# Kernel tuning notes

Measured on AMD Instinct MI355X. Metric: run time of the kernel, lower is better.

Reference implementation:

```python
import jax, jax.numpy as jnp
import numpy as np

N, E, B = 30000, 480000, 64
F_IN, HID, ED = 128, 64, 32
NEG, EPS = 0.2, 1e-5


def _add_self_loops(edge_index, edge_attr):
    # PyG add_self_loops with fill_value='mean': self-loop edge_attr of node i
    # is the mean of edge_attr over edges whose destination is i.
    src, dst = edge_index[0], edge_index[1]
    cnt = jax.ops.segment_sum(jnp.ones((edge_attr.shape[0],), edge_attr.dtype), dst, num_segments=N)
    mean = jax.ops.segment_sum(edge_attr, dst, num_segments=N) / jnp.maximum(cnt, 1.0)[:, None]
    loop = jnp.arange(N)
    return jnp.concatenate([src, loop]), jnp.concatenate([dst, loop]), jnp.concatenate([edge_attr, mean], axis=0)


def _gat_conv(x, src, dst, ea, W, We, a_s, a_d, a_e, bias, H, Fo):
    xs = (x @ W).reshape(-1, H, Fo)              # [N, H, Fo]
    al_src = (xs * a_s).sum(-1)                  # [N, H]
    al_dst = (xs * a_d).sum(-1)                  # [N, H]
    ef = (ea @ We).reshape(-1, H, Fo)            # [Et, H, Fo]
    alpha = al_src[src] + al_dst[dst] + (ef * a_e).sum(-1)   # [Et, H]
    alpha = jax.nn.leaky_relu(alpha, NEG)
    # softmax over incoming edges of each destination node (segment softmax)
    m = jax.ops.segment_max(alpha, dst, num_segments=N)
    ex = jnp.exp(alpha - m[dst])
    s = jax.ops.segment_sum(ex, dst, num_segments=N)
    w = ex / s[dst]                              # [Et, H]
    out = jax.ops.segment_sum(xs[src] * w[:, :, None], dst, num_segments=N)
    return out.reshape(-1, H * Fo) + bias


def _bn(x, g, b):
    # BatchNorm1d in training mode: biased batch statistics over nodes
    mu = x.mean(0)
    var = x.var(0)
    return (x - mu) * jax.lax.rsqrt(var + EPS) * g + b


def _pool(x, batch, Wg, bg):
    # GlobalAttention: softmax(gate_nn(x)) per graph, weighted sum of x
    gate = (x @ Wg + bg)[:, 0]                   # [N]
    m = jax.ops.segment_max(gate, batch, num_segments=B)
    e = jnp.exp(gate - m[batch])
    s = jax.ops.segment_sum(e, batch, num_segments=B)
    w = e / s[batch]
    return jax.ops.segment_sum(x * w[:, None], batch, num_segments=B)   # [B, HID]


def setup_inputs():
    k = jax.random.split(jax.random.key(0), 16)
    g = lambda i, shape, fan: jax.random.normal(k[i], shape, jnp.float32) / np.sqrt(fan)
    return {
        "x": jax.random.normal(k[0], (N, F_IN), jnp.float32),
        "edge_attr": jax.random.normal(k[1], (E, ED), jnp.float32),
        "edge_index": jax.random.randint(k[2], (2, E), 0, N),
        "batch": jnp.sort(jax.random.randint(k[3], (N,), 0, B)),
        "W1": g(4, (F_IN, 4 * HID), F_IN),
        "We1": g(5, (ED, 4 * HID), ED),
        "att_src1": g(6, (4, HID), HID),
        "att_dst1": g(7, (4, HID), HID),
        "att_edge1": g(8, (4, HID), HID),
        "bias1": jnp.zeros((4 * HID,), jnp.float32),
        "g1": jnp.ones((4 * HID,), jnp.float32),
        "b1": jnp.zeros((4 * HID,), jnp.float32),
        "W2": g(9, (4 * HID, HID), 4 * HID),
        "We2": g(10, (ED, HID), ED),
        "att_src2": g(11, (1, HID), HID),
        "att_dst2": g(12, (1, HID), HID),
        "att_edge2": g(13, (1, HID), HID),
        "bias2": jnp.zeros((HID,), jnp.float32),
        "g2": jnp.ones((HID,), jnp.float32),
        "b2": jnp.zeros((HID,), jnp.float32),
        "Wg": g(14, (HID, 1), HID),
        "bg": jnp.zeros((1,), jnp.float32),
    }


def reference(x, edge_attr, edge_index, batch, W1, We1, att_src1, att_dst1, att_edge1, bias1, g1, b1, W2, We2, att_src2, att_dst2, att_edge2, bias2, g2, b2, Wg, bg):
    src, dst, ea = _add_self_loops(edge_index, edge_attr)
    h = jax.nn.relu(_bn(_gat_conv(x, src, dst, ea, W1, We1, att_src1, att_dst1, att_edge1, bias1, 4, HID), g1, b1))
    h = jax.nn.relu(_bn(_gat_conv(h, src, dst, ea, W2, We2, att_src2, att_dst2, att_edge2, bias2, 1, HID), g2, b2))
    return _pool(h, batch, Wg, bg)
```

## Files before the change

### kernel.cpp

```cpp
#include <hip/hip_runtime.h>
#include <math.h>

#define NN 30000
#define EE 480000
#define BB 64

typedef __bf16 b16x8 __attribute__((ext_vector_type(8)));
typedef float  f32x4 __attribute__((ext_vector_type(4)));
typedef unsigned short u16x8 __attribute__((ext_vector_type(8)));

__device__ __forceinline__ float wsum64(float v){
  #pragma unroll
  for (int m = 32; m >= 1; m >>= 1) v += __shfl_xor(v, m, 64);
  return v;
}
__device__ __forceinline__ float wmax64(float v){
  #pragma unroll
  for (int m = 32; m >= 1; m >>= 1) v = fmaxf(v, __shfl_xor(v, m, 64));
  return v;
}
__device__ __forceinline__ float wsum16(float v){
  #pragma unroll
  for (int m = 1; m < 16; m <<= 1) v += __shfl_xor(v, m, 64);
  return v;
}
__device__ __forceinline__ unsigned short f2b(float f){
  union { float f; unsigned u; } v; v.f = f;
  unsigned r = v.u + 0x7fffu + ((v.u >> 16) & 1u);
  return (unsigned short)(r >> 16);
}
__device__ __forceinline__ float b2f(unsigned short u){
  union { unsigned u; float f; } v; v.u = ((unsigned)u) << 16;
  return v.f;
}

__global__ void hist_kernel(const int* __restrict__ dst, int* __restrict__ deg){
  int e = blockIdx.x*256 + threadIdx.x;
  if (e < EE) atomicAdd(&deg[dst[e]], 1);
}

__global__ __launch_bounds__(256) void scan_kernel(const int* __restrict__ deg, int* __restrict__ rowptr){
  __shared__ int s[256];
  __shared__ int wred[4];
  const int b = blockIdx.x, tid = threadIdx.x;
  const int base = b*256;
  int part = 0;
  for (int idx = tid; idx < base; idx += 256) part += deg[idx];
  #pragma unroll
  for (int m = 32; m >= 1; m >>= 1) part += __shfl_xor(part, m, 64);
  if ((tid & 63) == 0) wred[tid >> 6] = part;
  __syncthreads();
  int offset = wred[0] + wred[1] + wred[2] + wred[3];
  int n = base + tid;
  int d = (n < NN) ? deg[n] : 0;
  s[tid] = d;
  __syncthreads();
  for (int off = 1; off < 256; off <<= 1){
    int v = (tid >= off) ? s[tid - off] : 0;
    __syncthreads();
    s[tid] += v;
    __syncthreads();
  }
  if (n < NN) rowptr[n] = offset + s[tid] - d;
  if (b == 0 && tid == 0) rowptr[NN] = EE;
}

__global__ void prep_kernel(const float* __restrict__ W1, const float* __restrict__ W2,
                            const float* __restrict__ We1, const float* __restrict__ ae1,
                            const float* __restrict__ We2, const float* __restrict__ ae2,
                            unsigned short* __restrict__ W1t, unsigned short* __restrict__ W2t,
                            float* __restrict__ wae){
  int t = threadIdx.x, b = blockIdx.x;
  if (b < 128){
    W1t[t*128 + b] = f2b(W1[b*256 + t]);
  } else if (b < 384){
    int k = b - 128;
    if (t < 64) W2t[t*256 + k] = f2b(W2[k*64 + t]);
  } else {
    if (t < 128){
      int h = t >> 5, k = t & 31;
      float s = 0.f;
      for (int f = 0; f < 64; f++) s += We1[k*256 + h*64 + f] * ae1[h*64 + f];
      wae[h*32 + k] = s;
    } else if (t < 160){
      int k = t - 128;
      float s = 0.f;
      for (int f = 0; f < 64; f++) s += We2[k*64 + f] * ae2[f];
      wae[128 + k] = s;
    }
  }
}

__global__ __launch_bounds__(256) void edge_kernel(const float* __restrict__ ea,
    const float* __restrict__ wae, const int* __restrict__ src, const int* __restrict__ dst,
    const int* __restrict__ rowptr, int* __restrict__ cursor,
    float* __restrict__ rec, float2* __restrict__ rec8){
  __shared__ float s_w[160];
  if (threadIdx.x < 160) s_w[threadIdx.x] = wae[threadIdx.x];
  __syncthreads();
  const int lane = threadIdx.x & 63;
  const int il = lane & 7;
  const int e = blockIdx.x*32 + (threadIdx.x >> 3);
  if (e >= EE) return;
  int slot = 0, sv = 0;
  if (il == 0){
    int dd = dst[e];
    slot = rowptr[dd] + atomicAdd(&cursor[dd], 1);
    sv = src[e];
  }
  float4 v = *(const float4*)(ea + (size_t)e*32 + il*4);
  float dots[5];
  #pragma unroll
  for (int h = 0; h < 5; h++){
    float4 w = *(const float4*)&s_w[h*32 + il*4];
    dots[h] = v.x*w.x + v.y*w.y + v.z*w.z + v.w*w.w;
  }
  #pragma unroll
  for (int m = 1; m < 8; m <<= 1)
    #pragma unroll
    for (int h = 0; h < 5; h++) dots[h] += __shfl_xor(dots[h], m, 64);
  slot = __shfl(slot, lane & ~7, 64);
  sv   = __shfl(sv,   lane & ~7, 64);
  if (il == 0){
    float4 lo; lo.x = dots[0]; lo.y = dots[1]; lo.z = dots[2]; lo.w = dots[3];
    *(float4*)(rec + (size_t)slot*8) = lo;
  } else if (il == 1){
    float4 hi; hi.x = dots[4]; hi.y = __int_as_float(sv); hi.z = 0.f; hi.w = 0.f;
    *(float4*)(rec + (size_t)slot*8 + 4) = hi;
  } else if (il == 2){
    float2 r8; r8.x = dots[4]; r8.y = __int_as_float(sv);
    rec8[slot] = r8;
  }
}

__global__ __launch_bounds__(256) void gemm1_mfma(const float* __restrict__ x,
    const unsigned short* __restrict__ Bt, const float* __restrict__ a_s, const float* __restrict__ a_d,
    unsigned short* __restrict__ out, float* __restrict__ alsrc, float* __restrict__ aldst){
  __shared__ unsigned short As[128*136];
  __shared__ unsigned short Bs[64*136];
  const int tid = threadIdx.x;
  const int w = tid >> 6, lane = tid & 63;
  const int c = lane & 15, gq = lane >> 4;
  const int m0 = blockIdx.x * 128;
  const int h0 = blockIdx.y * 2;
  #pragma unroll
  for (int q = 0; q < 16; q++){
    int ch = tid*16 + q;
    int r = ch >> 5, off = (ch & 31)*4;
    int grow = m0 + r;
    ushort4 o;
    if (grow < NN){
      float4 v = *(const float4*)(x + (size_t)grow*128 + off);
      o.x = f2b(v.x); o.y = f2b(v.y); o.z = f2b(v.z); o.w = f2b(v.w);
    } else o = make_ushort4(0,0,0,0);
    *(ushort4*)&As[r*136 + off] = o;
  }
  #pragma unroll
  for (int q = 0; q < 4; q++){
    int ch = tid*4 + q;
    int n = ch >> 4, off = (ch & 15)*8;
    *(ulonglong2*)&Bs[n*136 + off] = *(const ulonglong2*)(Bt + (size_t)(h0*64 + n)*128 + off);
  }
  __syncthreads();
  for (int hi = 0; hi < 2; hi++){
    const int head = h0 + hi;
    f32x4 acc[2][4];
    #pragma unroll
    for (int mt = 0; mt < 2; mt++)
      #pragma unroll
      for (int nt = 0; nt < 4; nt++) acc[mt][nt] = (f32x4){0.f,0.f,0.f,0.f};
    #pragma unroll
    for (int k0 = 0; k0 < 128; k0 += 32){
      b16x8 afr[2], bfr[4];
      #pragma unroll
      for (int mt = 0; mt < 2; mt++)
        afr[mt] = *(const b16x8*)&As[(w*32 + mt*16 + c)*136 + k0 + gq*8];
      #pragma unroll
      for (int nt = 0; nt < 4; nt++)
        bfr[nt] = *(const b16x8*)&Bs[(nt*16 + c)*136 + k0 + gq*8];
      #pragma unroll
      for (int mt = 0; mt < 2; mt++)
        #pragma unroll
        for (int nt = 0; nt < 4; nt++)
          acc[mt][nt] = __builtin_amdgcn_mfma_f32_16x16x32_bf16(afr[mt], bfr[nt], acc[mt][nt], 0, 0, 0);
    }
    __syncthreads();
    if (hi == 0){
      #pragma unroll
      for (int q = 0; q < 4; q++){
        int ch = tid*4 + q;
        int n = ch >> 4, off = (ch & 15)*8;
        *(ulonglong2*)&Bs[n*136 + off] = *(const ulonglong2*)(Bt + (size_t)((h0+1)*64 + n)*128 + off);
      }
    }
    float asv[4], adv[4];
    #pragma unroll
    for (int nt = 0; nt < 4; nt++){
      asv[nt] = a_s[head*64 + nt*16 + c];
      adv[nt] = a_d[head*64 + nt*16 + c];
    }
    #pragma unroll
    for (int mt = 0; mt < 2; mt++){
      int base_row = m0 + w*32 + mt*16 + gq*4;
      #pragma unroll
      for (int r = 0; r < 4; r++){
        int row = base_row + r;
        float ps = 0.f, pd = 0.f;
        #pragma unroll
        for (int nt = 0; nt < 4; nt++){
          ps += acc[mt][nt][r] * asv[nt];
          pd += acc[mt][nt][r] * adv[nt];
        }
        ps = wsum16(ps); pd = wsum16(pd);
        if (row < NN){
          if (c == 0){
            alsrc[(size_t)row*4 + head] = ps;
            aldst[(size_t)row*4 + head] = pd;
          }
          #pragma unroll
          for (int nt = 0; nt < 4; nt++)
            out[(size_t)row*256 + head*64 + nt*16 + c] = f2b(acc[mt][nt][r]);
        }
      }
    }
    if (hi == 0) __syncthreads();
  }
}

__global__ __launch_bounds__(256) void gemm2_mfma(const unsigned short* __restrict__ Ab,
    const unsigned short* __restrict__ Bt,
    const float* __restrict__ cs, const float* __restrict__ csq,
    const float* __restrict__ g, const float* __restrict__ b,
    const float* __restrict__ a_s, const float* __restrict__ a_d,
    unsigned short* __restrict__ out, float* __restrict__ alsrc, float* __restrict__ aldst){
  __shared__ unsigned short As[128*136];
  __shared__ unsigned short Bs[64*136];
  __shared__ float s_scale[256], s_shift[256];
  const int tid = threadIdx.x;
  const int w = tid >> 6, lane = tid & 63;
  const int c = lane & 15, gq = lane >> 4;
  const int m0 = blockIdx.x * 128;
  {
    float mu  = cs[tid]  * (1.f/NN);
    float var = csq[tid] * (1.f/NN) - mu*mu;
    float rs  = rsqrtf(var + 1e-5f);
    float sc  = rs * g[tid];
    s_scale[tid] = sc;
    s_shift[tid] = b[tid] - mu*sc;
  }
  __syncthreads();
  f32x4 acc[2][4];
  #pragma unroll
  for (int mt = 0; mt < 2; mt++)
    #pragma unroll
    for (int nt = 0; nt < 4; nt++) acc[mt][nt] = (f32x4){0.f,0.f,0.f,0.f};
  for (int kp = 0; kp < 256; kp += 128){
    #pragma unroll
    for (int q = 0; q < 16; q++){
      int ch = tid*16 + q;
      int r = ch >> 5, off = (ch & 31)*4;
      int grow = m0 + r;
      ushort4 o;
      if (grow < NN){
        ushort4 v = *(const ushort4*)(Ab + (size_t)grow*256 + kp + off);
        float4 sc = *(const float4*)&s_scale[kp + off];
        float4 sh = *(const float4*)&s_shift[kp + off];
        o.x = f2b(fmaxf(fmaf(b2f(v.x), sc.x, sh.x), 0.f));
        o.y = f2b(fmaxf(fmaf(b2f(v.y), sc.y, sh.y), 0.f));
        o.z = f2b(fmaxf(fmaf(b2f(v.z), sc.z, sh.z), 0.f));
        o.w = f2b(fmaxf(fmaf(b2f(v.w), sc.w, sh.w), 0.f));
      } else o = make_ushort4(0,0,0,0);
      *(ushort4*)&As[r*136 + off] = o;
    }
    #pragma unroll
    for (int q = 0; q < 4; q++){
      int ch = tid*4 + q;
      int n = ch >> 4, off = (ch & 15)*8;
      *(ulonglong2*)&Bs[n*136 + off] = *(const ulonglong2*)(Bt + (size_t)n*256 + kp + off);
    }
    __syncthreads();
    #pragma unroll
    for (int k0 = 0; k0 < 128; k0 += 32){
      b16x8 afr[2], bfr[4];
      #pragma unroll
      for (int mt = 0; mt < 2; mt++)
        afr[mt] = *(const b16x8*)&As[(w*32 + mt*16 + c)*136 + k0 + gq*8];
      #pragma unroll
      for (int nt = 0; nt < 4; nt++)
        bfr[nt] = *(const b16x8*)&Bs[(nt*16 + c)*136 + k0 + gq*8];
      #pragma unroll
      for (int mt = 0; mt < 2; mt++)
        #pragma unroll
        for (int nt = 0; nt < 4; nt++)
          acc[mt][nt] = __builtin_amdgcn_mfma_f32_16x16x32_bf16(afr[mt], bfr[nt], acc[mt][nt], 0, 0, 0);
    }
    __syncthreads();
  }
  float asv[4], adv[4];
  #pragma unroll
  for (int nt = 0; nt < 4; nt++){
    asv[nt] = a_s[nt*16 + c];
    adv[nt] = a_d[nt*16 + c];
  }
  #pragma unroll
  for (int mt = 0; mt < 2; mt++){
    int base_row = m0 + w*32 + mt*16 + gq*4;
    #pragma unroll
    for (int r = 0; r < 4; r++){
      int row = base_row + r;
      float ps = 0.f, pd = 0.f;
      #pragma unroll
      for (int nt = 0; nt < 4; nt++){
        ps += acc[mt][nt][r] * asv[nt];
        pd += acc[mt][nt][r] * adv[nt];
      }
      ps = wsum16(ps); pd = wsum16(pd);
      if (row < NN){
        if (c == 0){
          alsrc[row] = ps;
          aldst[row] = pd;
        }
        #pragma unroll
        for (int nt = 0; nt < 4; nt++)
          out[(size_t)row*64 + nt*16 + c] = f2b(acc[mt][nt][r]);
      }
    }
  }
}

template<int H>
__global__ __launch_bounds__(256) void agg_kernel(const int* __restrict__ rowptr,
    const float* __restrict__ rec,
    const float* __restrict__ al_src, const float* __restrict__ al_dst,
    const unsigned short* __restrict__ xsb, const float* __restrict__ bias,
    unsigned short* __restrict__ outb, float* __restrict__ outf){
  constexpr int CH = 128;
  __shared__ float s_e_all[4][CH*H];
  __shared__ int   s_src_all[4][CH];
  const int wid  = threadIdx.x >> 6;
  const int lane = threadIdx.x & 63;
  const int i = blockIdx.x*4 + wid;
  float* s_e  = s_e_all[wid];
  int*   s_src = s_src_all[wid];
  const int r0 = rowptr[i];
  const int d  = rowptr[i+1] - r0;
  float ad[H], asi[H];
  #pragma unroll
  for (int h = 0; h < H; h++){ ad[h] = al_dst[(size_t)i*H+h]; asi[h] = al_src[(size_t)i*H+h]; }
  float sesum[H], m[H];
  #pragma unroll
  for (int h = 0; h < H; h++){ sesum[h] = 0.f; m[h] = -1e30f; }
  for (int t = lane; t < d; t += 64){
    float al[H];
    int sn;
    if constexpr (H == 4){
      const float* rp = rec + (size_t)(r0 + t)*8;
      float4 ev = *(const float4*)rp;
      float2 hi = *(const float2*)(rp + 4);
      sn = __float_as_int(hi.y);
      float4 av = *(const float4*)(al_src + (size_t)sn*4);
      al[0]=av.x+ad[0]+ev.x; al[1]=av.y+ad[1]+ev.y; al[2]=av.z+ad[2]+ev.z; al[3]=av.w+ad[3]+ev.w;
      sesum[0]+=ev.x; sesum[1]+=ev.y; sesum[2]+=ev.z; sesum[3]+=ev.w;
    } else {
      float2 hi = ((const float2*)rec)[r0 + t];
      sn = __float_as_int(hi.y);
      al[0] = al_src[sn] + ad[0] + hi.x;
      sesum[0] += hi.x;
    }
    if (t < CH) s_src[t] = sn;
    #pragma unroll
    for (int h = 0; h < H; h++){
      float a = al[h]; a = a > 0.f ? a : 0.2f*a;
      if (t < CH) s_e[t*H+h] = a;
      m[h] = fmaxf(m[h], a);
    }
  }
  float invd = (d > 0) ? 1.f/(float)d : 0.f;
  float sa[H];
  #pragma unroll
  for (int h = 0; h < H; h++){
    sesum[h] = wsum64(sesum[h]);
    m[h] = wmax64(m[h]);
    float a = asi[h] + ad[h] + sesum[h]*invd;
    sa[h] = a > 0.f ? a : 0.2f*a;
    m[h] = fmaxf(m[h], sa[h]);
  }
  float acc8[8];
  #pragma unroll
  for (int j = 0; j < 8; j++) acc8[j] = 0.f;
  float dpart[H];
  #pragma unroll
  for (int h = 0; h < H; h++) dpart[h] = 0.f;
  const int half = lane >> 5, il5 = lane & 31;
  const int grp  = lane >> 3, il3 = lane & 7;
  int c0 = 0;
  while (c0 < d){
    int cl = min(CH, d - c0);
    if (c0 > 0){
      for (int t = lane; t < cl; t += 64){
        if constexpr (H == 4){
          const float* rp = rec + (size_t)(r0 + c0 + t)*8;
          float4 ev = *(const float4*)rp;
          float2 hi = *(const float2*)(rp + 4);
          int sn = __float_as_int(hi.y);
          s_src[t] = sn;
          float4 av = *(const float4*)(al_src + (size_t)sn*4);
          float a0=av.x+ad[0]+ev.x, a1=av.y+ad[1]+ev.y, a2=av.z+ad[2]+ev.z, a3=av.w+ad[3]+ev.w;
          s_e[t*4+0]=a0>0.f?a0:0.2f*a0; s_e[t*4+1]=a1>0.f?a1:0.2f*a1;
          s_e[t*4+2]=a2>0.f?a2:0.2f*a2; s_e[t*4+3]=a3>0.f?a3:0.2f*a3;
        } else {
          float2 hi = ((const float2*)rec)[r0 + c0 + t];
          int sn = __float_as_int(hi.y);
          s_src[t] = sn;
          float a = al_src[sn] + ad[0] + hi.x;
          s_e[t] = a > 0.f ? a : 0.2f*a;
        }
      }
    }
    for (int t = lane; t < cl; t += 64){
      #pragma unroll
      for (int h = 0; h < H; h++){
        float e = __expf(s_e[t*H+h] - m[h]);
        s_e[t*H+h] = e;
        dpart[h] += e;
      }
    }
    __builtin_amdgcn_wave_barrier();
    if constexpr (H == 4){
      const int hd = il5 >> 3;
      for (int t = half; t < cl; t += 2){
        int sn = s_src[t];
        float wv = s_e[t*4 + hd];
        u16x8 u = *(const u16x8*)(xsb + (size_t)sn*256 + il5*8);
        #pragma unroll
        for (int j = 0; j < 8; j++) acc8[j] += wv * b2f(u[j]);
      }
    } else {
      for (int t = grp; t < cl; t += 8){
        int sn = s_src[t];
        float wv = s_e[t];
        u16x8 u = *(const u16x8*)(xsb + (size_t)sn*64 + il3*8);
        #pragma unroll
        for (int j = 0; j < 8; j++) acc8[j] += wv * b2f(u[j]);
      }
    }
    __builtin_amdgcn_wave_barrier();
    c0 += CH;
  }
  float es[H];
  #pragma unroll
  for (int h = 0; h < H; h++) es[h] = __expf(sa[h] - m[h]);
  if (lane == 0){
    #pragma unroll
    for (int h = 0; h < H; h++) dpart[h] += es[h];
  }
  if constexpr (H == 4){
    if (half == 0){
      float wv = es[il5 >> 3];
      u16x8 u = *(const u16x8*)(xsb + (size_t)i*256 + il5*8);
      #pragma unroll
      for (int j = 0; j < 8; j++) acc8[j] += wv * b2f(u[j]);
    }
  } else {
    if (grp == 0){
      float wv = es[0];
      u16x8 u = *(const u16x8*)(xsb + (size_t)i*64 + il3*8);
      #pragma unroll
      for (int j = 0; j < 8; j++) acc8[j] += wv * b2f(u[j]);
    }
  }
  float denom[H];
  #pragma unroll
  for (int h = 0; h < H; h++) denom[h] = wsum64(dpart[h]);
  if constexpr (H == 4){
    #pragma unroll
    for (int j = 0; j < 8; j++) acc8[j] += __shfl_xor(acc8[j], 32, 64);
    if (lane < 32){
      float inv = 1.f / denom[il5 >> 3];
      u16x8 o;
      #pragma unroll
      for (int j = 0; j < 8; j++) o[j] = f2b(acc8[j]*inv + bias[il5*8 + j]);
      *(u16x8*)(outb + (size_t)i*256 + il5*8) = o;
    }
  } else {
    #pragma unroll
    for (int j = 0; j < 8; j++){
      acc8[j] += __shfl_xor(acc8[j], 8, 64);
      acc8[j] += __shfl_xor(acc8[j], 16, 64);
      acc8[j] += __shfl_xor(acc8[j], 32, 64);
    }
    if (lane < 8){
      float inv = 1.f / denom[0];
      float4 o0, o1;
      o0.x = acc8[0]*inv + bias[il3*8+0]; o0.y = acc8[1]*inv + bias[il3*8+1];
      o0.z = acc8[2]*inv + bias[il3*8+2]; o0.w = acc8[3]*inv + bias[il3*8+3];
      o1.x = acc8[4]*inv + bias[il3*8+4]; o1.y = acc8[5]*inv + bias[il3*8+5];
      o1.z = acc8[6]*inv + bias[il3*8+6]; o1.w = acc8[7]*inv + bias[il3*8+7];
      *(float4*)(outf + (size_t)i*64 + il3*8)     = o0;
      *(float4*)(outf + (size_t)i*64 + il3*8 + 4) = o1;
    }
  }
}

__global__ __launch_bounds__(256) void bn_stats_b16_kernel(const unsigned short* __restrict__ h,
    float* __restrict__ cs, float* __restrict__ csq){
  __shared__ float s_red[4][256], q_red[4][256];
  const int tid = threadIdx.x;
  const int wv = tid >> 6, lane = tid & 63;
  const int rg = lane >> 5, cg = lane & 31;
  float s8[8], q8[8];
  #pragma unroll
  for (int j = 0; j < 8; j++){ s8[j] = 0.f; q8[j] = 0.f; }
  for (int chunk = blockIdx.x; chunk < 3750; chunk += 256){
    int r = chunk*8 + wv*2 + rg;
    u16x8 u = *(const u16x8*)(h + (size_t)r*256 + cg*8);
    #pragma unroll
    for (int j = 0; j < 8; j++){
      float v = b2f(u[j]);
      s8[j] += v; q8[j] += v*v;
    }
  }
  #pragma unroll
  for (int j = 0; j < 8; j++){
    s8[j] += __shfl_xor(s8[j], 32, 64);
    q8[j] += __shfl_xor(q8[j], 32, 64);
  }
  if (lane < 32){
    #pragma unroll
    for (int j = 0; j < 8; j++){
      s_red[wv][cg*8 + j] = s8[j];
      q_red[wv][cg*8 + j] = q8[j];
    }
  }
  __syncthreads();
  if (tid < 256){
    float ts = s_red[0][tid] + s_red[1][tid] + s_red[2][tid] + s_red[3][tid];
    float tq = q_red[0][tid] + q_red[1][tid] + q_red[2][tid] + q_red[3][tid];
    atomicAdd(&cs[tid], ts);
    atomicAdd(&csq[tid], tq);
  }
}

__global__ __launch_bounds__(256) void bn_stats_f32_kernel(const float* __restrict__ h,
    float* __restrict__ cs, float* __restrict__ csq){
  int col = threadIdx.x & 63;
  int ro  = threadIdx.x >> 6;
  float s = 0.f, s2 = 0.f;
  for (int r = blockIdx.x*4 + ro; r < NN; r += 1024){
    float v = h[(size_t)r*64 + col];
    s += v; s2 += v*v;
  }
  atomicAdd(&cs[col], s);
  atomicAdd(&csq[col], s2);
}

__global__ __launch_bounds__(256) void gate_kernel(const float* __restrict__ h,
    const float* __restrict__ cs, const float* __restrict__ csq,
    const float* __restrict__ g2, const float* __restrict__ b2,
    const float* __restrict__ Wg, const float* __restrict__ bg,
    float* __restrict__ gate){
  int wid = threadIdx.x >> 6, lane = threadIdx.x & 63;
  int n = blockIdx.x*4 + wid;
  float mu  = cs[lane]  * (1.f/NN);
  float var = csq[lane] * (1.f/NN) - mu*mu;
  float rs  = rsqrtf(var + 1e-5f);
  float sc  = rs * g2[lane];
  float sh  = b2[lane] - mu*sc;
  float v = h[(size_t)n*64 + lane];
  float xx = fmaxf(fmaf(v, sc, sh), 0.f);
  float p = wsum64(xx * Wg[lane]);
  if (lane == 0) gate[n] = p + bg[0];
}

__global__ __launch_bounds__(256) void pool_kernel(const int* __restrict__ batch,
    const float* __restrict__ gate, const float* __restrict__ h2,
    const float* __restrict__ cs, const float* __restrict__ csq,
    const float* __restrict__ g2, const float* __restrict__ b2,
    float* __restrict__ out){
  __shared__ float red[256];
  __shared__ float a_red[4][64], w_red[4];
  __shared__ int seb[2];
  int b = blockIdx.x, tid = threadIdx.x;
  int wv = tid >> 6, lane = tid & 63;
  if (tid < 2){
    int target = b + tid;
    int lo = 0, hi = NN;
    while (lo < hi){ int mid = (lo+hi) >> 1; if (batch[mid] < target) lo = mid+1; else hi = mid; }
    seb[tid] = lo;
  }
  __syncthreads();
  int s = seb[0], e = seb[1];
  if (e <= s){ if (tid < 64) out[b*64 + tid] = 0.f; return; }
  float mloc = -1e30f;
  for (int n = s + tid; n < e; n += 256) mloc = fmaxf(mloc, gate[n]);
  mloc = wmax64(mloc);
  if (lane == 0) red[wv] = mloc;
  __syncthreads();
  float m = fmaxf(fmaxf(red[0], red[1]), fmaxf(red[2], red[3]));
  int rgrp = tid >> 4, cq = tid & 15;
  float4 csv = *(const float4*)(cs + cq*4);
  float4 cqv = *(const float4*)(csq + cq*4);
  float4 gv  = *(const float4*)(g2 + cq*4);
  float4 bv  = *(const float4*)(b2 + cq*4);
  float4 scv, shv;
  {
    float mu0 = csv.x*(1.f/NN), mu1 = csv.y*(1.f/NN), mu2 = csv.z*(1.f/NN), mu3 = csv.w*(1.f/NN);
    scv.x = rsqrtf(cqv.x*(1.f/NN) - mu0*mu0 + 1e-5f) * gv.x;
    scv.y = rsqrtf(cqv.y*(1.f/NN) - mu1*mu1 + 1e-5f) * gv.y;
    scv.z = rsqrtf(cqv.z*(1.f/NN) - mu2*mu2 + 1e-5f) * gv.z;
    scv.w = rsqrtf(cqv.w*(1.f/NN) - mu3*mu3 + 1e-5f) * gv.w;
    shv.x = bv.x - mu0*scv.x; shv.y = bv.y - mu1*scv.y;
    shv.z = bv.z - mu2*scv.z; shv.w = bv.w - mu3*scv.w;
  }
  f32x4 acc = (f32x4){0.f,0.f,0.f,0.f};
  float wp = 0.f;
  for (int n = s + rgrp; n < e; n += 16){
    float wgt = __expf(gate[n] - m);
    float4 v = *(const float4*)(h2 + (size_t)n*64 + cq*4);
    acc[0] += wgt*fmaxf(fmaf(v.x, scv.x, shv.x), 0.f);
    acc[1] += wgt*fmaxf(fmaf(v.y, scv.y, shv.y), 0.f);
    acc[2] += wgt*fmaxf(fmaf(v.z, scv.z, shv.z), 0.f);
    acc[3] += wgt*fmaxf(fmaf(v.w, scv.w, shv.w), 0.f);
    if (cq == 0) wp += wgt;
  }
  #pragma unroll
  for (int j = 0; j < 4; j++){
    acc[j] += __shfl_xor(acc[j], 16, 64);
    acc[j] += __shfl_xor(acc[j], 32, 64);
  }
  wp += __shfl_xor(wp, 16, 64);
  wp += __shfl_xor(wp, 32, 64);
  if (lane < 16){
    #pragma unroll
    for (int j = 0; j < 4; j++) a_red[wv][lane*4 + j] = acc[j];
  }
  if (lane == 0) w_red[wv] = wp;
  __syncthreads();
  if (tid < 64){
    float tot = a_red[0][tid] + a_red[1][tid] + a_red[2][tid] + a_red[3][tid];
    float wsm = w_red[0] + w_red[1] + w_red[2] + w_red[3];
    out[b*64 + tid] = tot / wsm;
  }
}

extern "C" void kernel_launch(void* const* d_in, const int* in_sizes, int n_in,
                              void* d_out, int out_size, void* d_ws, size_t ws_size,
                              hipStream_t stream){
  const float* x     = (const float*)d_in[0];
  const float* ea    = (const float*)d_in[1];
  const int*   ei    = (const int*)d_in[2];
  const int*   batch = (const int*)d_in[3];
  const float* W1    = (const float*)d_in[4];
  const float* We1   = (const float*)d_in[5];
  const float* as1   = (const float*)d_in[6];
  const float* ad1   = (const float*)d_in[7];
  const float* ae1   = (const float*)d_in[8];
  const float* bias1 = (const float*)d_in[9];
  const float* g1    = (const float*)d_in[10];
  const float* b1    = (const float*)d_in[11];
  const float* W2    = (const float*)d_in[12];
  const float* We2   = (const float*)d_in[13];
  const float* as2   = (const float*)d_in[14];
  const float* ad2   = (const float*)d_in[15];
  const float* ae2   = (const float*)d_in[16];
  const float* bias2 = (const float*)d_in[17];
  const float* g2    = (const float*)d_in[18];
  const float* b2    = (const float*)d_in[19];
  const float* Wg    = (const float*)d_in[20];
  const float* bg    = (const float*)d_in[21];
  const int* srcI = ei;
  const int* dstI = ei + EE;

  char* ws = (char*)d_ws;
  int*   deg    = (int*)(ws + 0);
  int*   cursor = (int*)(ws + 120064);
  float* stats  = (float*)(ws + 240128);
  int*   rowptr = (int*)(ws + 244224);
  float* wae    = (float*)(ws + 364288);
  unsigned short* W1t = (unsigned short*)(ws + 365056);
  unsigned short* W2t = (unsigned short*)(ws + 430592);
  float* alsrc  = (float*)(ws + 463360);
  float* aldst  = (float*)(ws + 943360);
  float* gateb  = (float*)(ws + 1423360);
  float* rec    = (float*)(ws + 1543424);
  unsigned short* xs1b = (unsigned short*)(ws + 16903424);
  unsigned short* h1b  = (unsigned short*)(ws + 32263424);
  unsigned short* xs2b = (unsigned short*)(ws + 47623424);
  float* h2     = (float*)(ws + 51463424);
  float2* rec8  = (float2*)(ws + 59143424);

  (void)hipMemsetAsync(ws, 0, 244224, stream);

  hist_kernel<<<1875, 256, 0, stream>>>(dstI, deg);
  scan_kernel<<<118, 256, 0, stream>>>(deg, rowptr);
  prep_kernel<<<385, 256, 0, stream>>>(W1, W2, We1, ae1, We2, ae2, W1t, W2t, wae);
  edge_kernel<<<15000, 256, 0, stream>>>(ea, wae, srcI, dstI, rowptr, cursor, rec, rec8);

  gemm1_mfma<<<dim3(235, 2), 256, 0, stream>>>(x, W1t, as1, ad1, xs1b, alsrc, aldst);
  agg_kernel<4><<<7500, 256, 0, stream>>>(rowptr, rec, alsrc, aldst, xs1b, bias1, h1b, nullptr);
  bn_stats_b16_kernel<<<256, 256, 0, stream>>>(h1b, stats + 0, stats + 256);

  gemm2_mfma<<<235, 256, 0, stream>>>(h1b, W2t, stats + 0, stats + 256, g1, b1,
                                      as2, ad2, xs2b, alsrc, aldst);
  agg_kernel<1><<<7500, 256, 0, stream>>>(rowptr, (const float*)rec8, alsrc, aldst, xs2b, bias2, nullptr, h2);
  bn_stats_f32_kernel<<<256, 256, 0, stream>>>(h2, stats + 512, stats + 576);

  gate_kernel<<<7500, 256, 0, stream>>>(h2, stats + 512, stats + 576, g2, b2, Wg, bg, gateb);
  pool_kernel<<<64, 256, 0, stream>>>(batch, gateb, h2, stats + 512, stats + 576, g2, b2, (float*)d_out);
}
```

Baseline: 373.4 us.

## Fuse gate into pool, merge hist/prep, drop rec8, one gemm1 block per row tile

Folds the degree histogram into the weight-prep kernel and moves the gate computation into the pool kernel, caching per-node gates in shared memory. This removes two launches and the gate buffer round trip. The separate compact rec8 record array is dropped, so the layer-2 aggregation reads the strided 8-float records instead. gemm1 now computes all four heads per block, which halves the grid and the x staging work at the cost of less parallelism. The shared gate cache only holds 2048 nodes per graph; larger graphs would silently be wrong.

```diff
diff --git a/kernel.cpp b/kernel.cpp
--- a/kernel.cpp
+++ b/kernel.cpp
@@ -34,43 +34,20 @@
   return v.f;
 }
 
-__global__ void hist_kernel(const int* __restrict__ dst, int* __restrict__ deg){
-  int e = blockIdx.x*256 + threadIdx.x;
-  if (e < EE) atomicAdd(&deg[dst[e]], 1);
-}
-
-__global__ __launch_bounds__(256) void scan_kernel(const int* __restrict__ deg, int* __restrict__ rowptr){
-  __shared__ int s[256];
-  __shared__ int wred[4];
-  const int b = blockIdx.x, tid = threadIdx.x;
-  const int base = b*256;
-  int part = 0;
-  for (int idx = tid; idx < base; idx += 256) part += deg[idx];
-  #pragma unroll
-  for (int m = 32; m >= 1; m >>= 1) part += __shfl_xor(part, m, 64);
-  if ((tid & 63) == 0) wred[tid >> 6] = part;
-  __syncthreads();
-  int offset = wred[0] + wred[1] + wred[2] + wred[3];
-  int n = base + tid;
-  int d = (n < NN) ? deg[n] : 0;
-  s[tid] = d;
-  __syncthreads();
-  for (int off = 1; off < 256; off <<= 1){
-    int v = (tid >= off) ? s[tid - off] : 0;
-    __syncthreads();
-    s[tid] += v;
-    __syncthreads();
-  }
-  if (n < NN) rowptr[n] = offset + s[tid] - d;
-  if (b == 0 && tid == 0) rowptr[NN] = EE;
-}
-
-__global__ void prep_kernel(const float* __restrict__ W1, const float* __restrict__ W2,
+__global__ void hist_prep_kernel(const int* __restrict__ dst, int* __restrict__ deg,
+                            const float* __restrict__ W1, const float* __restrict__ W2,
                             const float* __restrict__ We1, const float* __restrict__ ae1,
                             const float* __restrict__ We2, const float* __restrict__ ae2,
                             unsigned short* __restrict__ W1t, unsigned short* __restrict__ W2t,
                             float* __restrict__ wae){
-  int t = threadIdx.x, b = blockIdx.x;
+  int t = threadIdx.x;
+  int b = blockIdx.x;
+  if (b < 1875){
+    int e = b*256 + t;
+    if (e < EE) atomicAdd(&deg[dst[e]], 1);
+    return;
+  }
+  b -= 1875;
   if (b < 128){
     W1t[t*128 + b] = f2b(W1[b*256 + t]);
   } else if (b < 384){
@@ -91,10 +68,35 @@
   }
 }
 
+__global__ __launch_bounds__(256) void scan_kernel(const int* __restrict__ deg, int* __restrict__ rowptr){
+  __shared__ int s[256];
+  __shared__ int wred[4];
+  const int b = blockIdx.x, tid = threadIdx.x;
+  const int base = b*256;
+  int part = 0;
+  for (int idx = tid; idx < base; idx += 256) part += deg[idx];
+  #pragma unroll
+  for (int m = 32; m >= 1; m >>= 1) part += __shfl_xor(part, m, 64);
+  if ((tid & 63) == 0) wred[tid >> 6] = part;
+  __syncthreads();
+  int offset = wred[0] + wred[1] + wred[2] + wred[3];
+  int n = base + tid;
+  int d = (n < NN) ? deg[n] : 0;
+  s[tid] = d;
+  __syncthreads();
+  for (int off = 1; off < 256; off <<= 1){
+    int v = (tid >= off) ? s[tid - off] : 0;
+    __syncthreads();
+    s[tid] += v;
+    __syncthreads();
+  }
+  if (n < NN) rowptr[n] = offset + s[tid] - d;
+  if (b == 0 && tid == 0) rowptr[NN] = EE;
+}
+
 __global__ __launch_bounds__(256) void edge_kernel(const float* __restrict__ ea,
     const float* __restrict__ wae, const int* __restrict__ src, const int* __restrict__ dst,
-    const int* __restrict__ rowptr, int* __restrict__ cursor,
-    float* __restrict__ rec, float2* __restrict__ rec8){
+    const int* __restrict__ rowptr, int* __restrict__ cursor, float* __restrict__ rec){
   __shared__ float s_w[160];
   if (threadIdx.x < 160) s_w[threadIdx.x] = wae[threadIdx.x];
   __syncthreads();
@@ -127,9 +129,6 @@
   } else if (il == 1){
     float4 hi; hi.x = dots[4]; hi.y = __int_as_float(sv); hi.z = 0.f; hi.w = 0.f;
     *(float4*)(rec + (size_t)slot*8 + 4) = hi;
-  } else if (il == 2){
-    float2 r8; r8.x = dots[4]; r8.y = __int_as_float(sv);
-    rec8[slot] = r8;
   }
 }
 
@@ -142,7 +141,6 @@
   const int w = tid >> 6, lane = tid & 63;
   const int c = lane & 15, gq = lane >> 4;
   const int m0 = blockIdx.x * 128;
-  const int h0 = blockIdx.y * 2;
   #pragma unroll
   for (int q = 0; q < 16; q++){
     int ch = tid*16 + q;
@@ -159,11 +157,10 @@
   for (int q = 0; q < 4; q++){
     int ch = tid*4 + q;
     int n = ch >> 4, off = (ch & 15)*8;
-    *(ulonglong2*)&Bs[n*136 + off] = *(const ulonglong2*)(Bt + (size_t)(h0*64 + n)*128 + off);
-  }
-  __syncthreads();
-  for (int hi = 0; hi < 2; hi++){
-    const int head = h0 + hi;
+    *(ulonglong2*)&Bs[n*136 + off] = *(const ulonglong2*)(Bt + (size_t)n*128 + off);
+  }
+  __syncthreads();
+  for (int head = 0; head < 4; head++){
     f32x4 acc[2][4];
     #pragma unroll
     for (int mt = 0; mt < 2; mt++)
@@ -185,12 +182,12 @@
           acc[mt][nt] = __builtin_amdgcn_mfma_f32_16x16x32_bf16(afr[mt], bfr[nt], acc[mt][nt], 0, 0, 0);
     }
     __syncthreads();
-    if (hi == 0){
+    if (head < 3){
       #pragma unroll
       for (int q = 0; q < 4; q++){
         int ch = tid*4 + q;
         int n = ch >> 4, off = (ch & 15)*8;
-        *(ulonglong2*)&Bs[n*136 + off] = *(const ulonglong2*)(Bt + (size_t)((h0+1)*64 + n)*128 + off);
+        *(ulonglong2*)&Bs[n*136 + off] = *(const ulonglong2*)(Bt + (size_t)((head+1)*64 + n)*128 + off);
       }
     }
     float asv[4], adv[4];
@@ -223,7 +220,7 @@
         }
       }
     }
-    if (hi == 0) __syncthreads();
+    if (head < 3) __syncthreads();
   }
 }
 
@@ -351,10 +348,10 @@
   #pragma unroll
   for (int h = 0; h < H; h++){ sesum[h] = 0.f; m[h] = -1e30f; }
   for (int t = lane; t < d; t += 64){
+    const float* rp = rec + (size_t)(r0 + t)*8;
     float al[H];
     int sn;
     if constexpr (H == 4){
-      const float* rp = rec + (size_t)(r0 + t)*8;
       float4 ev = *(const float4*)rp;
       float2 hi = *(const float2*)(rp + 4);
       sn = __float_as_int(hi.y);
@@ -362,7 +359,7 @@
       al[0]=av.x+ad[0]+ev.x; al[1]=av.y+ad[1]+ev.y; al[2]=av.z+ad[2]+ev.z; al[3]=av.w+ad[3]+ev.w;
       sesum[0]+=ev.x; sesum[1]+=ev.y; sesum[2]+=ev.z; sesum[3]+=ev.w;
     } else {
-      float2 hi = ((const float2*)rec)[r0 + t];
+      float2 hi = *(const float2*)(rp + 4);
       sn = __float_as_int(hi.y);
       al[0] = al_src[sn] + ad[0] + hi.x;
       sesum[0] += hi.x;
@@ -398,8 +395,8 @@
     int cl = min(CH, d - c0);
     if (c0 > 0){
       for (int t = lane; t < cl; t += 64){
+        const float* rp = rec + (size_t)(r0 + c0 + t)*8;
         if constexpr (H == 4){
-          const float* rp = rec + (size_t)(r0 + c0 + t)*8;
           float4 ev = *(const float4*)rp;
           float2 hi = *(const float2*)(rp + 4);
           int sn = __float_as_int(hi.y);
@@ -409,7 +406,7 @@
           s_e[t*4+0]=a0>0.f?a0:0.2f*a0; s_e[t*4+1]=a1>0.f?a1:0.2f*a1;
           s_e[t*4+2]=a2>0.f?a2:0.2f*a2; s_e[t*4+3]=a3>0.f?a3:0.2f*a3;
         } else {
-          float2 hi = ((const float2*)rec)[r0 + c0 + t];
+          float2 hi = *(const float2*)(rp + 4);
           int sn = __float_as_int(hi.y);
           s_src[t] = sn;
           float a = al_src[sn] + ad[0] + hi.x;
@@ -554,30 +551,14 @@
   atomicAdd(&csq[col], s2);
 }
 
-__global__ __launch_bounds__(256) void gate_kernel(const float* __restrict__ h,
+__global__ __launch_bounds__(256) void pool_kernel(const int* __restrict__ batch,
+    const float* __restrict__ h2,
     const float* __restrict__ cs, const float* __restrict__ csq,
     const float* __restrict__ g2, const float* __restrict__ b2,
     const float* __restrict__ Wg, const float* __restrict__ bg,
-    float* __restrict__ gate){
-  int wid = threadIdx.x >> 6, lane = threadIdx.x & 63;
-  int n = blockIdx.x*4 + wid;
-  float mu  = cs[lane]  * (1.f/NN);
-  float var = csq[lane] * (1.f/NN) - mu*mu;
-  float rs  = rsqrtf(var + 1e-5f);
-  float sc  = rs * g2[lane];
-  float sh  = b2[lane] - mu*sc;
-  float v = h[(size_t)n*64 + lane];
-  float xx = fmaxf(fmaf(v, sc, sh), 0.f);
-  float p = wsum64(xx * Wg[lane]);
-  if (lane == 0) gate[n] = p + bg[0];
-}
-
-__global__ __launch_bounds__(256) void pool_kernel(const int* __restrict__ batch,
-    const float* __restrict__ gate, const float* __restrict__ h2,
-    const float* __restrict__ cs, const float* __restrict__ csq,
-    const float* __restrict__ g2, const float* __restrict__ b2,
     float* __restrict__ out){
-  __shared__ float red[256];
+  __shared__ float s_gate[2048];
+  __shared__ float red[4];
   __shared__ float a_red[4][64], w_red[4];
   __shared__ int seb[2];
   int b = blockIdx.x, tid = threadIdx.x;
@@ -590,10 +571,23 @@
   }
   __syncthreads();
   int s = seb[0], e = seb[1];
-  if (e <= s){ if (tid < 64) out[b*64 + tid] = 0.f; return; }
+  int cnt = e - s;
+  if (cnt <= 0){ if (tid < 64) out[b*64 + tid] = 0.f; return; }
+  float mu  = cs[lane]  * (1.f/NN);
+  float var = csq[lane] * (1.f/NN) - mu*mu;
+  float sc  = rsqrtf(var + 1e-5f) * g2[lane];
+  float sh  = b2[lane] - mu*sc;
+  float wgv = Wg[lane];
+  float bgv = bg[0];
   float mloc = -1e30f;
-  for (int n = s + tid; n < e; n += 256) mloc = fmaxf(mloc, gate[n]);
-  mloc = wmax64(mloc);
+  for (int idx = wv; idx < cnt; idx += 4){
+    int n = s + idx;
+    float v = h2[(size_t)n*64 + lane];
+    float xx = fmaxf(fmaf(v, sc, sh), 0.f);
+    float p = wsum64(xx * wgv) + bgv;
+    if (lane == 0 && idx < 2048) s_gate[idx] = p;
+    mloc = fmaxf(mloc, p);
+  }
   if (lane == 0) red[wv] = mloc;
   __syncthreads();
   float m = fmaxf(fmaxf(red[0], red[1]), fmaxf(red[2], red[3]));
@@ -614,8 +608,9 @@
   }
   f32x4 acc = (f32x4){0.f,0.f,0.f,0.f};
   float wp = 0.f;
-  for (int n = s + rgrp; n < e; n += 16){
-    float wgt = __expf(gate[n] - m);
+  for (int idx = rgrp; idx < cnt; idx += 16){
+    int n = s + idx;
+    float wgt = __expf(s_gate[idx] - m);
     float4 v = *(const float4*)(h2 + (size_t)n*64 + cq*4);
     acc[0] += wgt*fmaxf(fmaf(v.x, scv.x, shv.x), 0.f);
     acc[1] += wgt*fmaxf(fmaf(v.y, scv.y, shv.y), 0.f);
@@ -681,30 +676,27 @@
   unsigned short* W2t = (unsigned short*)(ws + 430592);
   float* alsrc  = (float*)(ws + 463360);
   float* aldst  = (float*)(ws + 943360);
-  float* gateb  = (float*)(ws + 1423360);
   float* rec    = (float*)(ws + 1543424);
   unsigned short* xs1b = (unsigned short*)(ws + 16903424);
   unsigned short* h1b  = (unsigned short*)(ws + 32263424);
   unsigned short* xs2b = (unsigned short*)(ws + 47623424);
   float* h2     = (float*)(ws + 51463424);
-  float2* rec8  = (float2*)(ws + 59143424);
 
   (void)hipMemsetAsync(ws, 0, 244224, stream);
 
-  hist_kernel<<<1875, 256, 0, stream>>>(dstI, deg);
+  hist_prep_kernel<<<2260, 256, 0, stream>>>(dstI, deg, W1, W2, We1, ae1, We2, ae2, W1t, W2t, wae);
   scan_kernel<<<118, 256, 0, stream>>>(deg, rowptr);
-  prep_kernel<<<385, 256, 0, stream>>>(W1, W2, We1, ae1, We2, ae2, W1t, W2t, wae);
-  edge_kernel<<<15000, 256, 0, stream>>>(ea, wae, srcI, dstI, rowptr, cursor, rec, rec8);
-
-  gemm1_mfma<<<dim3(235, 2), 256, 0, stream>>>(x, W1t, as1, ad1, xs1b, alsrc, aldst);
+  edge_kernel<<<15000, 256, 0, stream>>>(ea, wae, srcI, dstI, rowptr, cursor, rec);
+
+  gemm1_mfma<<<235, 256, 0, stream>>>(x, W1t, as1, ad1, xs1b, alsrc, aldst);
   agg_kernel<4><<<7500, 256, 0, stream>>>(rowptr, rec, alsrc, aldst, xs1b, bias1, h1b, nullptr);
   bn_stats_b16_kernel<<<256, 256, 0, stream>>>(h1b, stats + 0, stats + 256);
 
   gemm2_mfma<<<235, 256, 0, stream>>>(h1b, W2t, stats + 0, stats + 256, g1, b1,
                                       as2, ad2, xs2b, alsrc, aldst);
-  agg_kernel<1><<<7500, 256, 0, stream>>>(rowptr, (const float*)rec8, alsrc, aldst, xs2b, bias2, nullptr, h2);
+  agg_kernel<1><<<7500, 256, 0, stream>>>(rowptr, rec, alsrc, aldst, xs2b, bias2, nullptr, h2);
   bn_stats_f32_kernel<<<256, 256, 0, stream>>>(h2, stats + 512, stats + 576);
 
-  gate_kernel<<<7500, 256, 0, stream>>>(h2, stats + 512, stats + 576, g2, b2, Wg, bg, gateb);
-  pool_kernel<<<64, 256, 0, stream>>>(batch, gateb, h2, stats + 512, stats + 576, g2, b2, (float*)d_out);
-}
+  pool_kernel<<<64, 256, 0, stream>>>(batch, h2, stats + 512, stats + 576, g2, b2, Wg, bg,
+                                      (float*)d_out);
+}
```

New measurement: 404.4 us. +8.3%, slower.
